# Kernel optimization log

Hardware: AMD Instinct MI355X
Metric: run time of the kernel (lower is better)

## Reference

```python
import jax, jax.numpy as jnp
import numpy as np

EMBED_DIM = 1024
NUM_HEADS = 16
HEAD_DIM = EMBED_DIM // NUM_HEADS
SCALE = HEAD_DIM ** -0.5


def setup_inputs() -> dict:
    key = jax.random.key(0)
    ks = jax.random.split(key, 5)
    B, N, D = 8, 1024, EMBED_DIM
    std = D ** -0.5
    x = jax.random.normal(ks[0], (B, N, D), dtype=jnp.float32)
    W_qkv = jax.random.normal(ks[1], (D, 3 * D), dtype=jnp.float32) * std
    b_qkv = jnp.zeros((3 * D,), dtype=jnp.float32)
    W_proj = jax.random.normal(ks[2], (D, D), dtype=jnp.float32) * std
    b_proj = jnp.zeros((D,), dtype=jnp.float32)
    return {"x": x, "W_qkv": W_qkv, "b_qkv": b_qkv, "W_proj": W_proj, "b_proj": b_proj}


def reference(x, W_qkv, b_qkv, W_proj, b_proj):
    B, N, D = x.shape
    H, hd = NUM_HEADS, HEAD_DIM
    # QKV projection: (B,N,3D) -> (3,B,H,N,hd)
    qkv = (x @ W_qkv + b_qkv).reshape(B, N, 3, H, hd).transpose(2, 0, 3, 1, 4)
    q, k, v = qkv[0], qkv[1], qkv[2]
    # scaled dot-product attention, full (B,H,N,N) scores as in original
    attn = jnp.einsum('bhqd,bhkd->bhqk', q, k) * SCALE
    attn = jax.nn.softmax(attn, axis=-1)
    out = jnp.einsum('bhqk,bhkd->bhqd', attn, v)  # (B,H,N,hd)
    out = out.transpose(0, 2, 1, 3).reshape(B, N, D)
    return out @ W_proj + b_proj
```

## Files before the change

### kernel.cpp

```cpp
#include <hip/hip_runtime.h>

#define AS1(p) ((const __attribute__((address_space(1))) void*)(p))
#define AS3(p) ((__attribute__((address_space(3))) void*)(p))

typedef __attribute__((ext_vector_type(8))) short bf16x8;
typedef __attribute__((ext_vector_type(4))) float f32x4;
typedef __attribute__((ext_vector_type(16))) float f32x16;

static constexpr int kBatch = 8;
static constexpr int kSeq = 1024;
static constexpr int kD = 1024;
static constexpr int kH = 16;
static constexpr int kHD = 64;
static constexpr int kRows = kBatch * kSeq;
static constexpr int kQKVCols = 3 * kD;

__device__ __forceinline__ unsigned short f2bf(float f) {
  union { float f; unsigned int u; } a; a.f = f;
  unsigned int r = a.u + 0x7fffu + ((a.u >> 16) & 1u);
  return (unsigned short)(r >> 16);
}

__device__ __forceinline__ unsigned pkbf(float a, float b) {
  unsigned r;
  asm("v_cvt_pk_bf16_f32 %0, %1, %2" : "=v"(r) : "v"(a), "v"(b));
  return r;
}

__global__ void cvt_bf16_kernel(const float* __restrict__ in,
                                unsigned short* __restrict__ out, int n4) {
  int i = blockIdx.x * blockDim.x + threadIdx.x;
  int stride = gridDim.x * blockDim.x;
  for (; i < n4; i += stride) {
    float4 v = reinterpret_cast<const float4*>(in)[i];
    ushort4 o;
    o.x = f2bf(v.x); o.y = f2bf(v.y); o.z = f2bf(v.z); o.w = f2bf(v.w);
    reinterpret_cast<ushort4*>(out)[i] = o;
  }
}

__global__ void transpose_cvt_kernel(const float* __restrict__ W,
                                     unsigned short* __restrict__ Wt,
                                     int rows, int cols) {
  __shared__ float tile[32][33];
  int c0 = blockIdx.x * 32, r0 = blockIdx.y * 32;
  int tx = threadIdx.x, ty = threadIdx.y;
#pragma unroll
  for (int i = 0; i < 32; i += 8)
    tile[ty + i][tx] = W[(size_t)(r0 + ty + i) * cols + (c0 + tx)];
  __syncthreads();
#pragma unroll
  for (int i = 0; i < 32; i += 8)
    Wt[(size_t)(c0 + ty + i) * rows + (r0 + tx)] = f2bf(tile[tx][ty + i]);
}

__device__ __forceinline__ int swap23(int x) {
  return (x & ~12) | ((x & 4) << 1) | ((x & 8) >> 1);
}
__global__ __launch_bounds__(256) void vtrans_kernel(
    const unsigned short* __restrict__ qkv, unsigned short* __restrict__ Vt) {
  __shared__ alignas(16) unsigned short tile[64][72];
  const int nt = blockIdx.x, bh = blockIdx.y;
  const int b = bh >> 4, h = bh & 15;
  const unsigned short* Vb = qkv + (size_t)b * kSeq * kQKVCols + 2 * kD + h * kHD;
  const int t = threadIdx.x;
#pragma unroll
  for (int r = 0; r < 2; ++r) {
    const int c = r * 256 + t;
    const int n = c >> 3, d8 = c & 7;
    uint4 v = *reinterpret_cast<const uint4*>(Vb + (size_t)(nt * 64 + n) * kQKVCols + d8 * 8);
    *reinterpret_cast<uint4*>(&tile[n][d8 * 8]) = v;
  }
  __syncthreads();
#pragma unroll
  for (int r = 0; r < 2; ++r) {
    const int c = r * 256 + t;
    const int d = c >> 3, n8 = c & 7;
    unsigned short w8[8];
#pragma unroll
    for (int j = 0; j < 8; ++j) w8[j] = tile[swap23(n8 * 8 + j)][d];
    *reinterpret_cast<uint4*>(Vt + (size_t)bh * kHD * kSeq + (size_t)d * kSeq + nt * 64 + n8 * 8) =
        *reinterpret_cast<uint4*>(w8);
  }
}

template <bool OUT_BF16>
__global__ __launch_bounds__(256) void gemm_bt_kernel(
    const unsigned short* __restrict__ A,
    const unsigned short* __restrict__ Bt,
    const float* __restrict__ bias,
    void* __restrict__ Cout, int M, int Nn, int K) {
  constexpr int BK = 64;
  __shared__ alignas(16) unsigned short As[128 * BK];
  __shared__ alignas(16) unsigned short Bs[128 * BK];
  const int t = threadIdx.x;
  const int lane = t & 63;
  const int w = t >> 6;
  const int wr = w >> 1, wc = w & 1;
  const int l15 = lane & 15, lhi = lane >> 4;
  const int nwg = gridDim.x * gridDim.y;
  const int lin = blockIdx.y * gridDim.x + blockIdx.x;
  const int swz = (lin & 7) * (nwg >> 3) + (lin >> 3);
  const int row0 = (swz / gridDim.x) * 128;
  const int col0 = (swz % gridDim.x) * 128;

  f32x4 acc[4][4] = {};
  const int ldsb = (t & ~63) * 16;

  for (int k0 = 0; k0 < K; k0 += BK) {
    __syncthreads();
#pragma unroll
    for (int r = 0; r < 4; ++r) {
      int c = r * 256 + t;
      int arow = c >> 3;
      int ccol = ((c & 7) ^ (arow & 7)) * 8;
      const unsigned short* ga = A + (size_t)(row0 + arow) * K + (k0 + ccol);
      const unsigned short* gb = Bt + (size_t)(col0 + arow) * K + (k0 + ccol);
      char* la = (char*)As + r * 4096 + ldsb;
      char* lb = (char*)Bs + r * 4096 + ldsb;
      __builtin_amdgcn_global_load_lds(AS1(ga), AS3(la), 16, 0, 0);
      __builtin_amdgcn_global_load_lds(AS1(gb), AS3(lb), 16, 0, 0);
    }
    __syncthreads();
#pragma unroll
    for (int kk = 0; kk < 2; ++kk) {
      bf16x8 af[4], bfr[4];
#pragma unroll
      for (int mi = 0; mi < 4; ++mi) {
        int rowa = wr * 64 + mi * 16 + l15;
        int chunk = (kk * 4 + lhi) ^ (rowa & 7);
        af[mi] = *reinterpret_cast<const bf16x8*>((const char*)As + rowa * 128 + chunk * 16);
      }
#pragma unroll
      for (int ni = 0; ni < 4; ++ni) {
        int rowb = wc * 64 + ni * 16 + l15;
        int chunk = (kk * 4 + lhi) ^ (rowb & 7);
        bfr[ni] = *reinterpret_cast<const bf16x8*>((const char*)Bs + rowb * 128 + chunk * 16);
      }
#pragma unroll
      for (int mi = 0; mi < 4; ++mi)
#pragma unroll
        for (int ni = 0; ni < 4; ++ni)
          acc[mi][ni] = __builtin_amdgcn_mfma_f32_16x16x32_bf16(af[mi], bfr[ni], acc[mi][ni], 0, 0, 0);
    }
  }
#pragma unroll
  for (int mi = 0; mi < 4; ++mi) {
    int rbase = row0 + wr * 64 + mi * 16 + lhi * 4;
#pragma unroll
    for (int ni = 0; ni < 4; ++ni) {
      int col = col0 + wc * 64 + ni * 16 + l15;
      float bv = bias[col];
#pragma unroll
      for (int j = 0; j < 4; ++j) {
        float v = acc[mi][ni][j] + bv;
        if (OUT_BF16)
          ((unsigned short*)Cout)[(size_t)(rbase + j) * Nn + col] = f2bf(v);
        else
          ((float*)Cout)[(size_t)(rbase + j) * Nn + col] = v;
      }
    }
  }
}

#define G256_STAGE_A(BUF, HALF, KT)                                           \
  do {                                                                        \
    char* _d = smem + (BUF) * 65536 + (HALF) * 16384 + ldst;                  \
    const unsigned short* _s0 = Ap + aoff0 + (size_t)(HALF) * halfstep + (KT) * 64; \
    const unsigned short* _s1 = Ap + aoff1 + (size_t)(HALF) * halfstep + (KT) * 64; \
    __builtin_amdgcn_global_load_lds(AS1(_s0), AS3(_d), 16, 0, 0);            \
    __builtin_amdgcn_global_load_lds(AS1(_s1), AS3(_d + 8192), 16, 0, 0);     \
  } while (0)
#define G256_STAGE_B(BUF, HALF, KT)                                           \
  do {                                                                        \
    char* _d = smem + (BUF) * 65536 + 32768 + (HALF) * 16384 + ldst;          \
    const unsigned short* _s0 = Bp + boff0 + (size_t)(HALF) * halfstep + (KT) * 64; \
    const unsigned short* _s1 = Bp + boff1 + (size_t)(HALF) * halfstep + (KT) * 64; \
    __builtin_amdgcn_global_load_lds(AS1(_s0), AS3(_d), 16, 0, 0);            \
    __builtin_amdgcn_global_load_lds(AS1(_s1), AS3(_d + 8192), 16, 0, 0);     \
  } while (0)
#define G256_PHASE(RBUF, QM, QN, STAGE_STMT, DO_VM)                           \
  do {                                                                        \
    const char* _Ab = smem + (RBUF) * 65536 + (QM) * 16384;                   \
    const char* _Bb = smem + (RBUF) * 65536 + 32768 + (QN) * 16384;           \
    bf16x8 _af[2][4], _bf[2][2];                                              \
    _Pragma("unroll") for (int kk = 0; kk < 2; ++kk) {                        \
      _Pragma("unroll") for (int mi = 0; mi < 4; ++mi) {                      \
        const int rr = wm * 64 + mi * 16 + l15;                               \
        const int ch = (kk * 4 + lhi) ^ (rr & 7);                             \
        _af[kk][mi] = *reinterpret_cast<const bf16x8*>(_Ab + rr * 128 + ch * 16); \
      }                                                                       \
      _Pragma("unroll") for (int ni = 0; ni < 2; ++ni) {                      \
        const int rr = wn * 32 + ni * 16 + l15;                               \
        const int ch = (kk * 4 + lhi) ^ (rr & 7);                             \
        _bf[kk][ni] = *reinterpret_cast<const bf16x8*>(_Bb + rr * 128 + ch * 16); \
      }                                                                       \
    }                                                                         \
    STAGE_STMT;                                                               \
    if (DO_VM) asm volatile("s_waitcnt vmcnt(4)" ::: "memory");               \
    asm volatile("" ::: "memory");                                            \
    __builtin_amdgcn_s_barrier();                                             \
    asm volatile("s_waitcnt lgkmcnt(0)" ::: "memory");                        \
    __builtin_amdgcn_sched_barrier(0);                                        \
    __builtin_amdgcn_s_setprio(1);                                            \
    _Pragma("unroll") for (int kk = 0; kk < 2; ++kk)                          \
      _Pragma("unroll") for (int mi = 0; mi < 4; ++mi)                        \
        _Pragma("unroll") for (int ni = 0; ni < 2; ++ni)                      \
          acc[QM][QN][mi][ni] = __builtin_amdgcn_mfma_f32_16x16x32_bf16(      \
              _af[kk][mi], _bf[kk][ni], acc[QM][QN][mi][ni], 0, 0, 0);        \
    __builtin_amdgcn_s_setprio(0);                                            \
    asm volatile("" ::: "memory");                                            \
    __builtin_amdgcn_s_barrier();                                             \
    asm volatile("" ::: "memory");                                            \
  } while (0)

template <bool OUT_BF16>
__global__ __launch_bounds__(512, 2) void gemm256_kernel(
    const unsigned short* __restrict__ Ap,
    const unsigned short* __restrict__ Bp,
    const float* __restrict__ bias,
    void* __restrict__ Cout, int M, int Nn, int K) {
  __shared__ alignas(16) char smem[131072];
  const int t = threadIdx.x;
  const int lane = t & 63;
  const int wid = t >> 6;
  const int wm = wid >> 2, wn = wid & 3;
  const int l15 = lane & 15, lhi = lane >> 4;

  const int nwg = gridDim.x * gridDim.y;
  const int lin = blockIdx.y * gridDim.x + blockIdx.x;
  const int swz = (lin & 7) * (nwg >> 3) + (lin >> 3);
  const int row0 = (swz / gridDim.x) * 256;
  const int col0 = (swz % gridDim.x) * 256;

  const int r0i = t >> 3, r1i = (512 + t) >> 3;
  const int sc0 = ((t & 7) ^ (r0i & 7)) * 8;
  const int sc1 = (((512 + t) & 7) ^ (r1i & 7)) * 8;
  const size_t aoff0 = (size_t)(row0 + r0i) * K + sc0;
  const size_t aoff1 = (size_t)(row0 + r1i) * K + sc1;
  const size_t boff0 = (size_t)(col0 + r0i) * K + sc0;
  const size_t boff1 = (size_t)(col0 + r1i) * K + sc1;
  const size_t halfstep = (size_t)128 * K;
  const int ldst = (t & ~63) * 16;

  f32x4 acc[2][2][4][2] = {};

  G256_STAGE_A(0, 0, 0);
  G256_STAGE_B(0, 1, 0);
  G256_STAGE_A(0, 1, 0);
  G256_STAGE_B(0, 0, 0);
  G256_STAGE_A(1, 0, 1);
  G256_STAGE_B(1, 1, 1);
  asm volatile("s_waitcnt vmcnt(4)" ::: "memory");
  __builtin_amdgcn_s_barrier();
  asm volatile("" ::: "memory");

  const int nkt = K >> 6;
  const int niter = nkt >> 1;
  for (int i = 0; i < niter; ++i) {
    const int tc1 = 2 * i + 1;
    const int tn0 = (2 * i + 2) & (nkt - 1);
    const int tn1 = (2 * i + 3) & (nkt - 1);
    G256_PHASE(0, 0, 0, G256_STAGE_A(1, 1, tc1), 0);
    G256_PHASE(0, 0, 1, G256_STAGE_B(1, 0, tc1), 0);
    G256_PHASE(0, 1, 1, G256_STAGE_A(0, 0, tn0), 0);
    G256_PHASE(0, 1, 0, G256_STAGE_B(0, 1, tn0), 1);
    G256_PHASE(1, 0, 0, G256_STAGE_A(0, 1, tn0), 0);
    G256_PHASE(1, 0, 1, G256_STAGE_B(0, 0, tn0), 0);
    G256_PHASE(1, 1, 1, G256_STAGE_A(1, 0, tn1), 0);
    G256_PHASE(1, 1, 0, G256_STAGE_B(1, 1, tn1), 1);
  }

#pragma unroll
  for (int qm = 0; qm < 2; ++qm)
#pragma unroll
    for (int mi = 0; mi < 4; ++mi) {
      const int rbase = row0 + qm * 128 + wm * 64 + mi * 16 + lhi * 4;
#pragma unroll
      for (int qn = 0; qn < 2; ++qn)
#pragma unroll
        for (int ni = 0; ni < 2; ++ni) {
          const int col = col0 + qn * 128 + wn * 32 + ni * 16 + l15;
          const float bv = bias[col];
#pragma unroll
          for (int j = 0; j < 4; ++j) {
            const float v = acc[qm][qn][mi][ni][j] + bv;
            if (OUT_BF16)
              ((unsigned short*)Cout)[(size_t)(rbase + j) * Nn + col] = f2bf(v);
            else
              ((float*)Cout)[(size_t)(rbase + j) * Nn + col] = v;
          }
        }
    }
}

__global__ __launch_bounds__(256) void attn_kernel(
    const unsigned short* __restrict__ qkv,
    const unsigned short* __restrict__ Vt,
    unsigned short* __restrict__ ctx) {
  __shared__ alignas(16) char smem[32768];
  const int qt = blockIdx.x >> 7;
  const int bh = blockIdx.x & 127;
  const int b = bh >> 4, h = bh & 15;
  const int t = threadIdx.x, lane = t & 63, w = t >> 6;
  const int l31 = lane & 31, hi = lane >> 5;

  const unsigned short* Qb = qkv + (size_t)b * kSeq * kQKVCols + h * kHD;
  const unsigned short* Kb = Qb + kD;
  const unsigned short* Vtb = Vt + (size_t)bh * kHD * kSeq;

  bf16x8 qf[4];
  const int qrow = qt * 128 + w * 32 + l31;
#pragma unroll
  for (int s = 0; s < 4; ++s)
    qf[s] = *reinterpret_cast<const bf16x8*>(Qb + (size_t)qrow * kQKVCols + s * 16 + hi * 8);

  auto stage = [&](int kt, int bufb) {
#pragma unroll
    for (int r = 0; r < 2; ++r) {
      const int c = r * 256 + t;
      const int row = c >> 3;
      const int sc = ((c & 7) ^ (row & 7)) * 8;
      const unsigned short* gk = Kb + (size_t)(kt * 64 + row) * kQKVCols + sc;
      const unsigned short* gv = Vtb + (size_t)row * kSeq + kt * 64 + sc;
      char* lk = smem + bufb + r * 4096 + (t & ~63) * 16;
      char* lv = smem + bufb + 8192 + r * 4096 + (t & ~63) * 16;
      __builtin_amdgcn_global_load_lds(AS1(gk), AS3(lk), 16, 0, 0);
      __builtin_amdgcn_global_load_lds(AS1(gv), AS3(lv), 16, 0, 0);
    }
  };

  f32x16 oacc[2] = {};
  float mrun = -3.0e38f, lrun = 0.f;
  constexpr float kSc = 0.125f * 1.44269504f;

  stage(0, 0);
  __syncthreads();
  int cur = 0;
  for (int kt = 0; kt < 16; ++kt) {
    if (kt < 15) stage(kt + 1, (cur ^ 1) * 16384);
    const char* Kp = smem + cur * 16384;
    const char* Vp = Kp + 8192;

    f32x16 sacc[2] = {};
    __builtin_amdgcn_s_setprio(1);
#pragma unroll
    for (int nb = 0; nb < 2; ++nb) {
      const int n = nb * 32 + l31;
#pragma unroll
      for (int s = 0; s < 4; ++s) {
        const int ch = (s * 2 + hi) ^ (n & 7);
        bf16x8 kf = *reinterpret_cast<const bf16x8*>(Kp + n * 128 + ch * 16);
        sacc[nb] = __builtin_amdgcn_mfma_f32_32x32x16_bf16(kf, qf[s], sacc[nb], 0, 0, 0);
      }
    }
    __builtin_amdgcn_s_setprio(0);

    float tm = sacc[0][0];
#pragma unroll
    for (int nb = 0; nb < 2; ++nb)
#pragma unroll
      for (int r = 0; r < 16; ++r) tm = fmaxf(tm, sacc[nb][r]);
    tm = fmaxf(tm, __shfl_xor(tm, 32, 64));
    const float tms = tm * kSc;
    if (!__all(tms <= mrun + 8.0f)) {
      const float mnew = fmaxf(mrun, tms);
      const float corr = __builtin_amdgcn_exp2f(mrun - mnew);
      mrun = mnew;
      lrun *= corr;
#pragma unroll
      for (int db = 0; db < 2; ++db)
#pragma unroll
        for (int r = 0; r < 16; ++r) oacc[db][r] *= corr;
    }
    float ps = 0.f;
#pragma unroll
    for (int nb = 0; nb < 2; ++nb)
#pragma unroll
      for (int r = 0; r < 16; ++r) {
        const float e = __builtin_amdgcn_exp2f(__builtin_fmaf(sacc[nb][r], kSc, -mrun));
        sacc[nb][r] = e;
        ps += e;
      }
    lrun += ps + __shfl_xor(ps, 32, 64);

    bf16x8 pf[4];
#pragma unroll
    for (int s = 0; s < 4; ++s) {
      const int nb = s >> 1, h2 = (s & 1) * 8;
      union { unsigned u[4]; bf16x8 v; } pk4;
#pragma unroll
      for (int i = 0; i < 4; ++i)
        pk4.u[i] = pkbf(sacc[nb][h2 + 2 * i], sacc[nb][h2 + 2 * i + 1]);
      pf[s] = pk4.v;
    }

    __builtin_amdgcn_s_setprio(1);
#pragma unroll
    for (int db = 0; db < 2; ++db) {
      const int dr = db * 32 + l31;
#pragma unroll
      for (int s = 0; s < 4; ++s) {
        const int ch = (s * 2 + hi) ^ (dr & 7);
        bf16x8 vf = *reinterpret_cast<const bf16x8*>(Vp + dr * 128 + ch * 16);
        oacc[db] = __builtin_amdgcn_mfma_f32_32x32x16_bf16(vf, pf[s], oacc[db], 0, 0, 0);
      }
    }
    __builtin_amdgcn_s_setprio(0);
    __syncthreads();
    cur ^= 1;
  }

  const float rl = 1.0f / lrun;
  const int qlocal = w * 32 + l31;
#pragma unroll
  for (int db = 0; db < 2; ++db)
#pragma unroll
    for (int g = 0; g < 4; ++g) {
      const unsigned u0 = pkbf(oacc[db][g * 4 + 0] * rl, oacc[db][g * 4 + 1] * rl);
      const unsigned u1 = pkbf(oacc[db][g * 4 + 2] * rl, oacc[db][g * 4 + 3] * rl);
      const int ch = db * 4 + g;
      uint2 uu; uu.x = u0; uu.y = u1;
      *reinterpret_cast<uint2*>(smem + qlocal * 128 + ((ch ^ (qlocal & 7)) * 16) + hi * 8) = uu;
    }
  __syncthreads();
#pragma unroll
  for (int it = 0; it < 4; ++it) {
    const int idx = it * 256 + t;
    const int row = idx >> 3, ch = idx & 7;
    const uint4 vv = *reinterpret_cast<const uint4*>(smem + row * 128 + ((ch ^ (row & 7)) * 16));
    *reinterpret_cast<uint4*>(ctx + (size_t)(b * kSeq + qt * 128 + row) * kD + h * kHD + ch * 8) = vv;
  }
}

extern "C" void kernel_launch(void* const* d_in, const int* in_sizes, int n_in,
                              void* d_out, int out_size, void* d_ws, size_t ws_size,
                              hipStream_t stream) {
  const float* x     = (const float*)d_in[0];
  const float* Wqkv  = (const float*)d_in[1];
  const float* bqkv  = (const float*)d_in[2];
  const float* Wproj = (const float*)d_in[3];
  const float* bproj = (const float*)d_in[4];
  float* out = (float*)d_out;

  char* ws = (char*)d_ws;
  size_t oXbf   = 0;
  size_t oWqkvT = oXbf   + (size_t)kRows * kD * 2;
  size_t oWpT   = oWqkvT + (size_t)kQKVCols * kD * 2;
  size_t oQKV   = oWpT   + (size_t)kD * kD * 2;
  size_t oCTX   = oQKV   + (size_t)kRows * kQKVCols * 2;
  size_t total  = oCTX   + (size_t)kRows * kD * 2;
  if (ws_size < total) return;

  unsigned short* Xbf   = (unsigned short*)(ws + oXbf);
  unsigned short* Vtb   = (unsigned short*)(ws + oXbf);
  unsigned short* WqkvT = (unsigned short*)(ws + oWqkvT);
  unsigned short* WpT   = (unsigned short*)(ws + oWpT);
  unsigned short* QKV   = (unsigned short*)(ws + oQKV);
  unsigned short* CTX   = (unsigned short*)(ws + oCTX);

  cvt_bf16_kernel<<<2048, 256, 0, stream>>>(x, Xbf, kRows * kD / 4);
  transpose_cvt_kernel<<<dim3(kQKVCols / 32, kD / 32), dim3(32, 8), 0, stream>>>(Wqkv, WqkvT, kD, kQKVCols);
  transpose_cvt_kernel<<<dim3(kD / 32, kD / 32), dim3(32, 8), 0, stream>>>(Wproj, WpT, kD, kD);
  gemm256_kernel<true><<<dim3(kQKVCols / 256, kRows / 256), 512, 0, stream>>>(
      Xbf, WqkvT, bqkv, QKV, kRows, kQKVCols, kD);
  vtrans_kernel<<<dim3(16, 128), 256, 0, stream>>>(QKV, Vtb);
  attn_kernel<<<1024, 256, 0, stream>>>(QKV, Vtb, CTX);
  gemm_bt_kernel<false><<<dim3(kD / 128, kRows / 128), 256, 0, stream>>>(
      CTX, WpT, bproj, out, kRows, kD, kD);
}
```

Before: 170.1 us.

## Fuse prep kernels and write transposed V directly from a split QKV GEMM

```diff
diff --git a/kernel.cpp b/kernel.cpp
--- a/kernel.cpp
+++ b/kernel.cpp
@@ -27,36 +27,48 @@
   return r;
 }
 
-__global__ void cvt_bf16_kernel(const float* __restrict__ in,
-                                unsigned short* __restrict__ out, int n4) {
-  int i = blockIdx.x * blockDim.x + threadIdx.x;
-  int stride = gridDim.x * blockDim.x;
-  for (; i < n4; i += stride) {
-    float4 v = reinterpret_cast<const float4*>(in)[i];
-    ushort4 o;
-    o.x = f2bf(v.x); o.y = f2bf(v.y); o.z = f2bf(v.z); o.w = f2bf(v.w);
-    reinterpret_cast<ushort4*>(out)[i] = o;
-  }
-}
-
-__global__ void transpose_cvt_kernel(const float* __restrict__ W,
-                                     unsigned short* __restrict__ Wt,
-                                     int rows, int cols) {
+__device__ __forceinline__ int swap23(int x) {
+  return (x & ~12) | ((x & 4) << 1) | ((x & 8) >> 1);
+}
+
+__global__ __launch_bounds__(256) void prep_kernel(
+    const float* __restrict__ x, unsigned short* __restrict__ Xbf,
+    const float* __restrict__ Wqkv, unsigned short* __restrict__ WqkvT,
+    const float* __restrict__ Wproj, unsigned short* __restrict__ WpT) {
+  const int bid = blockIdx.x, t = threadIdx.x;
+  if (bid < 1024) {
+    const int n4 = kRows * kD / 4;
+    int i = bid * 256 + t;
+    const int stride = 1024 * 256;
+    for (; i < n4; i += stride) {
+      float4 v = reinterpret_cast<const float4*>(x)[i];
+      ushort4 o;
+      o.x = f2bf(v.x); o.y = f2bf(v.y); o.z = f2bf(v.z); o.w = f2bf(v.w);
+      reinterpret_cast<ushort4*>(Xbf)[i] = o;
+    }
+    return;
+  }
   __shared__ float tile[32][33];
-  int c0 = blockIdx.x * 32, r0 = blockIdx.y * 32;
-  int tx = threadIdx.x, ty = threadIdx.y;
+  const float* W; unsigned short* Wt; int cols, c0, r0;
+  if (bid < 4096) {
+    const int idx = bid - 1024;
+    W = Wqkv; Wt = WqkvT; cols = kQKVCols;
+    c0 = (idx % 96) * 32; r0 = (idx / 96) * 32;
+  } else {
+    const int idx = bid - 4096;
+    W = Wproj; Wt = WpT; cols = kD;
+    c0 = (idx % 32) * 32; r0 = (idx / 32) * 32;
+  }
+  const int tx = t & 31, ty = t >> 5;
 #pragma unroll
   for (int i = 0; i < 32; i += 8)
     tile[ty + i][tx] = W[(size_t)(r0 + ty + i) * cols + (c0 + tx)];
   __syncthreads();
 #pragma unroll
   for (int i = 0; i < 32; i += 8)
-    Wt[(size_t)(c0 + ty + i) * rows + (r0 + tx)] = f2bf(tile[tx][ty + i]);
-}
-
-__device__ __forceinline__ int swap23(int x) {
-  return (x & ~12) | ((x & 4) << 1) | ((x & 8) >> 1);
-}
+    Wt[(size_t)(c0 + ty + i) * 1024 + (r0 + tx)] = f2bf(tile[tx][ty + i]);
+}
+
 __global__ __launch_bounds__(256) void vtrans_kernel(
     const unsigned short* __restrict__ qkv, unsigned short* __restrict__ Vt) {
   __shared__ alignas(16) unsigned short tile[64][72];
@@ -84,12 +96,13 @@
   }
 }
 
-template <bool OUT_BF16>
+template <int MODE>
 __global__ __launch_bounds__(256) void gemm_bt_kernel(
     const unsigned short* __restrict__ A,
     const unsigned short* __restrict__ Bt,
     const float* __restrict__ bias,
-    void* __restrict__ Cout, int M, int Nn, int K) {
+    void* __restrict__ Cout, unsigned short* __restrict__ Vt,
+    int M, int Nn, int K) {
   constexpr int BK = 64;
   __shared__ alignas(16) unsigned short As[128 * BK];
   __shared__ alignas(16) unsigned short Bs[128 * BK];
@@ -144,6 +157,28 @@
           acc[mi][ni] = __builtin_amdgcn_mfma_f32_16x16x32_bf16(af[mi], bfr[ni], acc[mi][ni], 0, 0, 0);
     }
   }
+
+  if (MODE == 3) {
+#pragma unroll
+    for (int mi = 0; mi < 4; ++mi) {
+      const int rbase = row0 + wr * 64 + mi * 16 + lhi * 4;
+      const int b = rbase >> 10, n = rbase & 1023;
+      const int nbase = (n & ~63) | swap23(n & 63);
+#pragma unroll
+      for (int ni = 0; ni < 4; ++ni) {
+        const int col = col0 + wc * 64 + ni * 16 + l15;
+        const int hv = col >> 6;
+        const int d = col & 63;
+        const float bv = bias[col];
+        uint2 uu;
+        uu.x = pkbf(acc[mi][ni][0] + bv, acc[mi][ni][1] + bv);
+        uu.y = pkbf(acc[mi][ni][2] + bv, acc[mi][ni][3] + bv);
+        *reinterpret_cast<uint2*>(Vt + ((size_t)((b << 4) + hv) << 16) + d * 1024 + nbase) = uu;
+      }
+    }
+    return;
+  }
+
 #pragma unroll
   for (int mi = 0; mi < 4; ++mi) {
     int rbase = row0 + wr * 64 + mi * 16 + lhi * 4;
@@ -154,7 +189,7 @@
 #pragma unroll
       for (int j = 0; j < 4; ++j) {
         float v = acc[mi][ni][j] + bv;
-        if (OUT_BF16)
+        if (MODE != 0)
           ((unsigned short*)Cout)[(size_t)(rbase + j) * Nn + col] = f2bf(v);
         else
           ((float*)Cout)[(size_t)(rbase + j) * Nn + col] = v;
@@ -214,12 +249,11 @@
     asm volatile("" ::: "memory");                                            \
   } while (0)
 
-template <bool OUT_BF16>
 __global__ __launch_bounds__(512, 2) void gemm256_kernel(
     const unsigned short* __restrict__ Ap,
     const unsigned short* __restrict__ Bp,
     const float* __restrict__ bias,
-    void* __restrict__ Cout, int M, int Nn, int K) {
+    unsigned short* __restrict__ Cout, int M, int Nn, int K) {
   __shared__ alignas(16) char smem[131072];
   const int t = threadIdx.x;
   const int lane = t & 63;
@@ -285,10 +319,7 @@
 #pragma unroll
           for (int j = 0; j < 4; ++j) {
             const float v = acc[qm][qn][mi][ni][j] + bv;
-            if (OUT_BF16)
-              ((unsigned short*)Cout)[(size_t)(rbase + j) * Nn + col] = f2bf(v);
-            else
-              ((float*)Cout)[(size_t)(rbase + j) * Nn + col] = v;
+            Cout[(size_t)(rbase + j) * Nn + col] = f2bf(v);
           }
         }
     }
@@ -449,23 +480,34 @@
   size_t oWpT   = oWqkvT + (size_t)kQKVCols * kD * 2;
   size_t oQKV   = oWpT   + (size_t)kD * kD * 2;
   size_t oCTX   = oQKV   + (size_t)kRows * kQKVCols * 2;
-  size_t total  = oCTX   + (size_t)kRows * kD * 2;
-  if (ws_size < total) return;
+  size_t oVt    = oCTX   + (size_t)kRows * kD * 2;
+  size_t total_base  = oVt;
+  size_t total_fused = oVt + (size_t)kRows * kD * 2;
+  if (ws_size < total_base) return;
+  const bool fused_vt = ws_size >= total_fused;
 
   unsigned short* Xbf   = (unsigned short*)(ws + oXbf);
-  unsigned short* Vtb   = (unsigned short*)(ws + oXbf);
   unsigned short* WqkvT = (unsigned short*)(ws + oWqkvT);
   unsigned short* WpT   = (unsigned short*)(ws + oWpT);
   unsigned short* QKV   = (unsigned short*)(ws + oQKV);
   unsigned short* CTX   = (unsigned short*)(ws + oCTX);
-
-  cvt_bf16_kernel<<<2048, 256, 0, stream>>>(x, Xbf, kRows * kD / 4);
-  transpose_cvt_kernel<<<dim3(kQKVCols / 32, kD / 32), dim3(32, 8), 0, stream>>>(Wqkv, WqkvT, kD, kQKVCols);
-  transpose_cvt_kernel<<<dim3(kD / 32, kD / 32), dim3(32, 8), 0, stream>>>(Wproj, WpT, kD, kD);
-  gemm256_kernel<true><<<dim3(kQKVCols / 256, kRows / 256), 512, 0, stream>>>(
-      Xbf, WqkvT, bqkv, QKV, kRows, kQKVCols, kD);
-  vtrans_kernel<<<dim3(16, 128), 256, 0, stream>>>(QKV, Vtb);
-  attn_kernel<<<1024, 256, 0, stream>>>(QKV, Vtb, CTX);
-  gemm_bt_kernel<false><<<dim3(kD / 128, kRows / 128), 256, 0, stream>>>(
-      CTX, WpT, bproj, out, kRows, kD, kD);
-}
+  unsigned short* VtF   = (unsigned short*)(ws + oVt);
+  unsigned short* VtA   = (unsigned short*)(ws + oXbf);
+
+  prep_kernel<<<5120, 256, 0, stream>>>(x, Xbf, Wqkv, WqkvT, Wproj, WpT);
+  if (fused_vt) {
+    gemm256_kernel<<<dim3(2048 / 256, kRows / 256), 512, 0, stream>>>(
+        Xbf, WqkvT, bqkv, QKV, kRows, kQKVCols, kD);
+    gemm_bt_kernel<3><<<dim3(1024 / 128, kRows / 128), 256, 0, stream>>>(
+        Xbf, WqkvT + (size_t)2048 * kD, bqkv + 2048, nullptr, VtF,
+        kRows, 1024, kD);
+    attn_kernel<<<1024, 256, 0, stream>>>(QKV, VtF, CTX);
+  } else {
+    gemm_bt_kernel<1><<<dim3(kQKVCols / 128, kRows / 128), 256, 0, stream>>>(
+        Xbf, WqkvT, bqkv, QKV, nullptr, kRows, kQKVCols, kD);
+    vtrans_kernel<<<dim3(16, 128), 256, 0, stream>>>(QKV, VtA);
+    attn_kernel<<<1024, 256, 0, stream>>>(QKV, VtA, CTX);
+  }
+  gemm_bt_kernel<0><<<dim3(kD / 128, kRows / 128), 256, 0, stream>>>(
+      CTX, WpT, bproj, out, nullptr, kRows, kD, kD);
+}
```

After: 156.6 us. 7.9% less time.
